# Optimization experiments

Measured on AMD Instinct MI355X. Metric: run time of the kernel, lower is better.

## Reference

```python
import jax, jax.numpy as jnp
import numpy as np

B, L, E, IN_A, IN_B, OUT = 32, 4096, 1024, 1024, 1024, 64
CACHE_LEN = 2048


def setup_inputs() -> dict:
    key = jax.random.key(0)
    ks = jax.random.split(key, 8)
    s = lambda n: 1.0 / np.sqrt(n)
    return {
        "inputA": jax.random.normal(ks[0], (B, IN_A), dtype=jnp.float32),
        "inputB": jax.random.normal(ks[1], (B, IN_B), dtype=jnp.float32),
        "cache": jnp.zeros((B, L, E), dtype=jnp.float32),
        "W1a": jax.random.normal(ks[2], (E, IN_A), dtype=jnp.float32) * s(IN_A),
        "b1a": jax.random.normal(ks[3], (E,), dtype=jnp.float32) * s(IN_A),
        "W1b": jax.random.normal(ks[4], (E, IN_B), dtype=jnp.float32) * s(IN_B),
        "b1b": jax.random.normal(ks[5], (E,), dtype=jnp.float32) * s(IN_B),
        "W2": jax.random.normal(ks[6], (OUT, E), dtype=jnp.float32) * s(E),
        "b2": jax.random.normal(ks[7], (OUT,), dtype=jnp.float32) * s(E),
        "cache_len": CACHE_LEN,
    }


def reference(inputA, inputB, cache, W1a, b1a, W1b, b1b, W2, b2, cache_len):
    # dual small Linear + add -> [B, E]
    vec = inputA @ W1a.T + b1a + inputB @ W1b.T + b1b
    # dynamic-index cache write (torch does this under no_grad)
    new_cache = cache.at[:, cache_len].set(jax.lax.stop_gradient(vec))
    # dynamic-length slice [B, cache_len+1, E], then output projection
    sliced = new_cache[:, : cache_len + 1]
    out = sliced @ W2.T + b2  # [B, cache_len+1, OUT]
    return out, new_cache
```

## Files before the change

kernel.cpp:

```cpp
#include <hip/hip_runtime.h>

#define Bq   32
#define Lq   4096
#define Eq   1024
#define OUTq 64
#define NW   16
#define TG   8

__global__ __launch_bounds__(256) void vec_kernel(
    const float* __restrict__ inA, const float* __restrict__ inB,
    const float* __restrict__ W1a, const float* __restrict__ b1a,
    const float* __restrict__ W1b, const float* __restrict__ b1b,
    float* __restrict__ vec)
{
    int wid  = (blockIdx.x * blockDim.x + threadIdx.x) >> 6;
    int lane = threadIdx.x & 63;
    int b    = wid & (Bq - 1);
    int e0   = (wid >> 5) << 3;
    if (e0 >= Eq) return;

    const float4* a4  = (const float4*)(inA + (size_t)b * Eq);
    const float4* bb4 = (const float4*)(inB + (size_t)b * Eq);
    float4 ar[4], br[4];
#pragma unroll
    for (int j = 0; j < 4; ++j) { ar[j] = a4[lane + 64 * j]; br[j] = bb4[lane + 64 * j]; }

#pragma unroll
    for (int k = 0; k < 8; ++k) {
        int e = e0 + k;
        const float4* wa = (const float4*)(W1a + (size_t)e * Eq);
        const float4* wb = (const float4*)(W1b + (size_t)e * Eq);
        float acc = 0.f;
#pragma unroll
        for (int j = 0; j < 4; ++j) {
            float4 w = wa[lane + 64 * j];
            acc += ar[j].x * w.x + ar[j].y * w.y + ar[j].z * w.z + ar[j].w * w.w;
            float4 v = wb[lane + 64 * j];
            acc += br[j].x * v.x + br[j].y * v.y + br[j].z * v.z + br[j].w * v.w;
        }
#pragma unroll
        for (int s = 32; s; s >>= 1) acc += __shfl_xor(acc, s, 64);
        if (lane == 0) vec[(size_t)b * Eq + e] = acc + b1a[e] + b1b[e];
    }
}

__global__ __launch_bounds__(256) void copy_kernel(
    const float* __restrict__ src, float* __restrict__ dst,
    int start_row, int f4_per_b)
{
    int b = blockIdx.y;
    int base = blockIdx.x * 1024 + threadIdx.x;
    size_t rowbase = ((size_t)b * Lq + start_row) * (Eq / 4);
    const float4* s4 = (const float4*)src;
    float4* d4 = (float4*)dst;
#pragma unroll
    for (int j = 0; j < 4; ++j) {
        int r4 = base + j * 256;
        if (r4 < f4_per_b) d4[rowbase + r4] = s4[rowbase + r4];
    }
}

__global__ __launch_bounds__(1024) void mm_kernel(
    const float* __restrict__ cache, const float* __restrict__ vec,
    const float* __restrict__ W2, const float* __restrict__ b2,
    float* __restrict__ outp, float* __restrict__ ncache, int cache_len)
{
    const int rows_per_b = cache_len + 1;
    const int total_rows = Bq * rows_per_b;
    const int n_groups = (total_rows + TG - 1) / TG;

    __shared__ float rowbuf[TG][Eq];
    __shared__ float part[NW][TG * 64];

    const int tid = threadIdx.x;
    const int w = tid >> 6, lane = tid & 63;

    float4 w2r[16];
#pragma unroll
    for (int j = 0; j < 16; ++j)
        w2r[j] = *(const float4*)(W2 + (size_t)lane * Eq + 64 * w + 4 * j);

    const int rsub = tid >> 7;
    const int c    = tid & 127;

    auto load_group = [&](int gg, float4& l0, float4& l1) {
        int row = gg * TG + rsub;
        if (row >= total_rows) row = total_rows - 1;
        int bb = row / rows_per_b;
        int t  = row - bb * rows_per_b;
        const float* src = (t == cache_len) ? (vec + (size_t)bb * Eq)
                                            : (cache + ((size_t)bb * Lq + t) * Eq);
        l0 = *(const float4*)(src + 4 * c);
        l1 = *(const float4*)(src + 4 * (c + 128));
    };

    int g = blockIdx.x;
    float4 ld0, ld1;
    if (g < n_groups) load_group(g, ld0, ld1);

    for (; g < n_groups; g += gridDim.x) {
        int row = g * TG + rsub;
        if (row < total_rows) {
            int bb = row / rows_per_b;
            int t  = row - bb * rows_per_b;
            float* dst = ncache + ((size_t)bb * Lq + t) * Eq;
            *(float4*)(dst + 4 * c)         = ld0;
            *(float4*)(dst + 4 * (c + 128)) = ld1;
        }
        *(float4*)(&rowbuf[rsub][4 * c])         = ld0;
        *(float4*)(&rowbuf[rsub][4 * (c + 128)]) = ld1;

        int gn = g + gridDim.x;
        if (gn < n_groups) load_group(gn, ld0, ld1);

        __syncthreads();

#pragma unroll
        for (int r = 0; r < TG; ++r) {
            float acc = 0.f;
#pragma unroll
            for (int j = 0; j < 16; ++j) {
                float4 rv = *(const float4*)(&rowbuf[r][64 * w + 4 * j]);
                acc += rv.x * w2r[j].x + rv.y * w2r[j].y +
                       rv.z * w2r[j].z + rv.w * w2r[j].w;
            }
            part[w][r * 64 + lane] = acc;
        }
        __syncthreads();

        if (tid < TG * 64) {
            float s = 0.f;
#pragma unroll
            for (int ww = 0; ww < NW; ++ww) s += part[ww][tid];
            int rr = tid >> 6, o = tid & 63;
            int row2 = g * TG + rr;
            if (row2 < total_rows) {
                int bb = row2 / rows_per_b;
                int t  = row2 - bb * rows_per_b;
                outp[((size_t)bb * rows_per_b + t) * OUTq + o] = s + b2[o];
            }
        }
        __syncthreads();
    }
}

extern "C" void kernel_launch(void* const* d_in, const int* in_sizes, int n_in,
                              void* d_out, int out_size, void* d_ws, size_t ws_size,
                              hipStream_t stream)
{
    const float* inA   = (const float*)d_in[0];
    const float* inB   = (const float*)d_in[1];
    const float* cache = (const float*)d_in[2];
    const float* W1a   = (const float*)d_in[3];
    const float* b1a   = (const float*)d_in[4];
    const float* W1b   = (const float*)d_in[5];
    const float* b1b   = (const float*)d_in[6];
    const float* W2    = (const float*)d_in[7];
    const float* b2v   = (const float*)d_in[8];

    float* outp = (float*)d_out;
    int rows_per_b = (out_size - Bq * Lq * Eq) / (Bq * OUTq);
    int cache_len  = rows_per_b - 1;
    float* ncache  = outp + (size_t)Bq * rows_per_b * OUTq;
    float* vec     = (float*)d_ws;

    vec_kernel<<<dim3(1024), dim3(256), 0, stream>>>(inA, inB, W1a, b1a, W1b, b1b, vec);

    int start_row = cache_len + 1;
    int f4_per_b  = (Lq - start_row) * (Eq / 4);
    if (f4_per_b > 0) {
        dim3 cg((f4_per_b + 1023) / 1024, Bq);
        copy_kernel<<<cg, dim3(256), 0, stream>>>(cache, ncache, start_row, f4_per_b);
    }

    mm_kernel<<<dim3(256), dim3(1024), 0, stream>>>(cache, vec, W2, b2v,
                                                    outp, ncache, cache_len);
}
```

Measured before the change: 294.8 us.

## Fuse tail cache copy into projection kernel and restructure vec GEMV

Removes the separate copy kernel and has each block of the projection kernel also copy the trailing cache rows past cache_len, with one batch per group of 8 blocks. The vec kernel is reorganised so each wavefront holds one weight row in registers and loops over the batch, reading each W1 row once. The trailing __syncthreads is dropped and the other barriers become raw s_waitcnt lgkmcnt plus s_barrier. This saves a launch and overlaps the bulk copy with the matmul, but the looser barriers risk LDS races between iterations and the copy work may be uneven across blocks if cache_len changes.

```diff
diff --git a/kernel.cpp b/kernel.cpp
--- a/kernel.cpp
+++ b/kernel.cpp
@@ -13,107 +13,107 @@
     const float* __restrict__ W1b, const float* __restrict__ b1b,
     float* __restrict__ vec)
 {
-    int wid  = (blockIdx.x * blockDim.x + threadIdx.x) >> 6;
+    int wid  = (blockIdx.x * 256 + threadIdx.x) >> 6;
     int lane = threadIdx.x & 63;
-    int b    = wid & (Bq - 1);
-    int e0   = (wid >> 5) << 3;
-    if (e0 >= Eq) return;
+    if (wid >= Eq) return;
+    int e = wid;
 
-    const float4* a4  = (const float4*)(inA + (size_t)b * Eq);
-    const float4* bb4 = (const float4*)(inB + (size_t)b * Eq);
-    float4 ar[4], br[4];
+    const float4* wa4 = (const float4*)(W1a + (size_t)e * Eq);
+    const float4* wb4 = (const float4*)(W1b + (size_t)e * Eq);
+    float4 wa[4], wb[4];
 #pragma unroll
-    for (int j = 0; j < 4; ++j) { ar[j] = a4[lane + 64 * j]; br[j] = bb4[lane + 64 * j]; }
+    for (int j = 0; j < 4; ++j) { wa[j] = wa4[lane + 64 * j]; wb[j] = wb4[lane + 64 * j]; }
+    float bias = b1a[e] + b1b[e];
 
-#pragma unroll
-    for (int k = 0; k < 8; ++k) {
-        int e = e0 + k;
-        const float4* wa = (const float4*)(W1a + (size_t)e * Eq);
-        const float4* wb = (const float4*)(W1b + (size_t)e * Eq);
+#pragma unroll 4
+    for (int b = 0; b < Bq; ++b) {
+        const float4* a4  = (const float4*)(inA + (size_t)b * Eq);
+        const float4* bb4 = (const float4*)(inB + (size_t)b * Eq);
         float acc = 0.f;
 #pragma unroll
         for (int j = 0; j < 4; ++j) {
-            float4 w = wa[lane + 64 * j];
-            acc += ar[j].x * w.x + ar[j].y * w.y + ar[j].z * w.z + ar[j].w * w.w;
-            float4 v = wb[lane + 64 * j];
-            acc += br[j].x * v.x + br[j].y * v.y + br[j].z * v.z + br[j].w * v.w;
+            float4 a = a4[lane + 64 * j];
+            acc += wa[j].x * a.x + wa[j].y * a.y + wa[j].z * a.z + wa[j].w * a.w;
+            float4 v = bb4[lane + 64 * j];
+            acc += wb[j].x * v.x + wb[j].y * v.y + wb[j].z * v.z + wb[j].w * v.w;
         }
 #pragma unroll
         for (int s = 32; s; s >>= 1) acc += __shfl_xor(acc, s, 64);
-        if (lane == 0) vec[(size_t)b * Eq + e] = acc + b1a[e] + b1b[e];
+        if (lane == 0) vec[(size_t)b * Eq + e] = acc + bias;
     }
 }
 
-__global__ __launch_bounds__(256) void copy_kernel(
-    const float* __restrict__ src, float* __restrict__ dst,
-    int start_row, int f4_per_b)
-{
-    int b = blockIdx.y;
-    int base = blockIdx.x * 1024 + threadIdx.x;
-    size_t rowbase = ((size_t)b * Lq + start_row) * (Eq / 4);
-    const float4* s4 = (const float4*)src;
-    float4* d4 = (float4*)dst;
-#pragma unroll
-    for (int j = 0; j < 4; ++j) {
-        int r4 = base + j * 256;
-        if (r4 < f4_per_b) d4[rowbase + r4] = s4[rowbase + r4];
-    }
-}
-
-__global__ __launch_bounds__(1024) void mm_kernel(
+__global__ __launch_bounds__(1024, 4) void fused_kernel(
     const float* __restrict__ cache, const float* __restrict__ vec,
     const float* __restrict__ W2, const float* __restrict__ b2,
-    float* __restrict__ outp, float* __restrict__ ncache, int cache_len)
+    float* __restrict__ outp, float* __restrict__ ncache,
+    int cache_len, int ngg, int ncg)
 {
-    const int rows_per_b = cache_len + 1;
-    const int total_rows = Bq * rows_per_b;
-    const int n_groups = (total_rows + TG - 1) / TG;
+    const int rows_out = cache_len + 1;
+    const int tid = threadIdx.x;
+    const int w = tid >> 6, lane = tid & 63;
+    const int b   = blockIdx.x >> 3;
+    const int blk = blockIdx.x & 7;
 
     __shared__ float rowbuf[TG][Eq];
     __shared__ float part[NW][TG * 64];
-
-    const int tid = threadIdx.x;
-    const int w = tid >> 6, lane = tid & 63;
 
     float4 w2r[16];
 #pragma unroll
     for (int j = 0; j < 16; ++j)
         w2r[j] = *(const float4*)(W2 + (size_t)lane * Eq + 64 * w + 4 * j);
 
+    const float bias = b2[tid & 63];
+
     const int rsub = tid >> 7;
     const int c    = tid & 127;
 
-    auto load_group = [&](int gg, float4& l0, float4& l1) {
-        int row = gg * TG + rsub;
-        if (row >= total_rows) row = total_rows - 1;
-        int bb = row / rows_per_b;
-        int t  = row - bb * rows_per_b;
-        const float* src = (t == cache_len) ? (vec + (size_t)bb * Eq)
-                                            : (cache + ((size_t)bb * Lq + t) * Eq);
-        l0 = *(const float4*)(src + 4 * c);
-        l1 = *(const float4*)(src + 4 * (c + 128));
+    const float* cb = cache  + (size_t)b * Lq * Eq;
+    float*       nb = ncache + (size_t)b * Lq * Eq;
+    const float* vb = vec    + (size_t)b * Eq;
+
+    float4 gld0 = {0,0,0,0}, gld1 = {0,0,0,0}, cld0 = {0,0,0,0}, cld1 = {0,0,0,0};
+
+    auto fetch_g = [&](int g) {
+        int t = TG * g + rsub;
+        if (g < ngg && t <= cache_len) {
+            const float* src = (t == cache_len) ? vb : (cb + (size_t)t * Eq);
+            gld0 = *(const float4*)(src + 4 * c);
+            gld1 = *(const float4*)(src + 4 * (c + 128));
+        }
+    };
+    auto fetch_c = [&](int cg) {
+        int t = rows_out + TG * cg + rsub;
+        if (cg < ncg && t < Lq) {
+            const float* src = cb + (size_t)t * Eq;
+            cld0 = *(const float4*)(src + 4 * c);
+            cld1 = *(const float4*)(src + 4 * (c + 128));
+        }
     };
 
-    int g = blockIdx.x;
-    float4 ld0, ld1;
-    if (g < n_groups) load_group(g, ld0, ld1);
+    fetch_g(blk);
+    fetch_c(blk);
 
-    for (; g < n_groups; g += gridDim.x) {
-        int row = g * TG + rsub;
-        if (row < total_rows) {
-            int bb = row / rows_per_b;
-            int t  = row - bb * rows_per_b;
-            float* dst = ncache + ((size_t)bb * Lq + t) * Eq;
-            *(float4*)(dst + 4 * c)         = ld0;
-            *(float4*)(dst + 4 * (c + 128)) = ld1;
+    for (int g = blk; g < ngg; g += 8) {
+        int t = TG * g + rsub;
+        if (t <= cache_len) {
+            float* dst = nb + (size_t)t * Eq;
+            *(float4*)(dst + 4 * c)          = gld0;
+            *(float4*)(dst + 4 * (c + 128))  = gld1;
+            *(float4*)(&rowbuf[rsub][4 * c])         = gld0;
+            *(float4*)(&rowbuf[rsub][4 * (c + 128)]) = gld1;
         }
-        *(float4*)(&rowbuf[rsub][4 * c])         = ld0;
-        *(float4*)(&rowbuf[rsub][4 * (c + 128)]) = ld1;
+        int tc = rows_out + TG * g + rsub;
+        if (g < ncg && tc < Lq) {
+            float* dst = nb + (size_t)tc * Eq;
+            *(float4*)(dst + 4 * c)         = cld0;
+            *(float4*)(dst + 4 * (c + 128)) = cld1;
+        }
 
-        int gn = g + gridDim.x;
-        if (gn < n_groups) load_group(gn, ld0, ld1);
+        fetch_g(g + 8);
+        fetch_c(g + 8);
 
-        __syncthreads();
+        asm volatile("s_waitcnt lgkmcnt(0)\n\ts_barrier" ::: "memory");
 
 #pragma unroll
         for (int r = 0; r < TG; ++r) {
@@ -126,21 +126,19 @@
             }
             part[w][r * 64 + lane] = acc;
         }
-        __syncthreads();
+
+        asm volatile("s_waitcnt lgkmcnt(0)\n\ts_barrier" ::: "memory");
 
         if (tid < TG * 64) {
-            float s = 0.f;
+            int rr = tid >> 6, o = tid & 63;
+            int trow = TG * g + rr;
+            if (trow < rows_out) {
+                float s = 0.f;
 #pragma unroll
-            for (int ww = 0; ww < NW; ++ww) s += part[ww][tid];
-            int rr = tid >> 6, o = tid & 63;
-            int row2 = g * TG + rr;
-            if (row2 < total_rows) {
-                int bb = row2 / rows_per_b;
-                int t  = row2 - bb * rows_per_b;
-                outp[((size_t)bb * rows_per_b + t) * OUTq + o] = s + b2[o];
+                for (int ww = 0; ww < NW; ++ww) s += part[ww][tid];
+                outp[((size_t)b * rows_out + trow) * OUTq + o] = s + bias;
             }
         }
-        __syncthreads();
     }
 }
 
@@ -159,20 +157,17 @@
     const float* b2v   = (const float*)d_in[8];
 
     float* outp = (float*)d_out;
-    int rows_per_b = (out_size - Bq * Lq * Eq) / (Bq * OUTq);
-    int cache_len  = rows_per_b - 1;
-    float* ncache  = outp + (size_t)Bq * rows_per_b * OUTq;
-    float* vec     = (float*)d_ws;
+    int rows_out  = (out_size - Bq * Lq * Eq) / (Bq * OUTq);
+    int cache_len = rows_out - 1;
+    float* ncache = outp + (size_t)Bq * rows_out * OUTq;
+    float* vecbuf = (float*)d_ws;
 
-    vec_kernel<<<dim3(1024), dim3(256), 0, stream>>>(inA, inB, W1a, b1a, W1b, b1b, vec);
+    int ngg = (rows_out + TG - 1) / TG;
+    int ncg = (Lq - rows_out + TG - 1) / TG;
 
-    int start_row = cache_len + 1;
-    int f4_per_b  = (Lq - start_row) * (Eq / 4);
-    if (f4_per_b > 0) {
-        dim3 cg((f4_per_b + 1023) / 1024, Bq);
-        copy_kernel<<<cg, dim3(256), 0, stream>>>(cache, ncache, start_row, f4_per_b);
-    }
+    vec_kernel<<<dim3(256), dim3(256), 0, stream>>>(inA, inB, W1a, b1a, W1b, b1b, vecbuf);
 
-    mm_kernel<<<dim3(256), dim3(1024), 0, stream>>>(cache, vec, W2, b2v,
-                                                    outp, ncache, cache_len);
+    fused_kernel<<<dim3(256), dim3(1024), 0, stream>>>(cache, vecbuf, W2, b2v,
+                                                       outp, ncache,
+                                                       cache_len, ngg, ncg);
 }
```

Measured after the change: 350.1 us. 1.19x slower.
